# Kernel tuning notes

Hardware: AMD Instinct MI355X
Metric: run time of the kernel (lower is better)

Reference implementation:

```python
import jax, jax.numpy as jnp
import numpy as np
from jax import lax

N_BITS = 4  # init kwarg n_bits
Q_SCALE = 2.0 ** (N_BITS - 1) - 1.0  # signed n-bit levels


def ste_round(x):
    # straight-through rounding (identity gradient)
    return x + lax.stop_gradient(jnp.round(x) - x)


def quant_signed(x):
    # clip to [-1,1], quantize to 2^(n-1)-1 signed levels with STE
    return ste_round(jnp.clip(x, -1.0, 1.0) * Q_SCALE) / Q_SCALE


def qconv(x, w):
    # QuantizeConv: 3x3 stride-1 pad-1 conv with n-bit quantized weights
    return lax.conv_general_dilated(x, quant_signed(w), window_strides=(1, 1),
                                    padding=((1, 1), (1, 1)),
                                    dimension_numbers=('NCHW', 'OIHW', 'NCHW'))


def qact_conv(x, g, b):
    # QuantizeSignedActSBN (conv): per-channel scale/bias then signed quant
    return quant_signed(x * g[None, :, None, None] + b[None, :, None, None])


def qact_fc(x, g, b):
    return quant_signed(x * g[None, :] + b[None, :])


def maxpool2(x):
    return lax.reduce_window(x, -jnp.inf, lax.max, (1, 1, 2, 2), (1, 1, 2, 2), 'VALID')


def setup_inputs() -> dict:
    key = jax.random.key(0)
    ks = jax.random.split(key, 32)
    B = 512
    x = jax.random.normal(ks[0], (B, 3, 32, 32), dtype=jnp.float32)
    chans = [(64, 3), (64, 64), (128, 64), (128, 128), (256, 128), (256, 256)]
    inp = {'x': x}
    ki = 1
    for i, (co, ci) in enumerate(chans, start=1):
        inp[f'w{i}'] = jax.random.normal(ks[ki], (co, ci, 3, 3), dtype=jnp.float32) * 0.05; ki += 1
        inp[f'g{i}'] = jax.random.uniform(ks[ki], (co,), dtype=jnp.float32, minval=0.5, maxval=1.5); ki += 1
        inp[f'b{i}'] = jax.random.normal(ks[ki], (co,), dtype=jnp.float32) * 0.05; ki += 1
    # FC head: 4096 -> 512 -> 10 (torch Linear weight layout [out, in])
    inp['wf1'] = jax.random.normal(ks[ki], (512, 4096), dtype=jnp.float32) * 0.02; ki += 1
    inp['gf1'] = jax.random.uniform(ks[ki], (512,), dtype=jnp.float32, minval=0.5, maxval=1.5); ki += 1
    inp['bf1'] = jax.random.normal(ks[ki], (512,), dtype=jnp.float32) * 0.05; ki += 1
    inp['wf2'] = jax.random.normal(ks[ki], (10, 512), dtype=jnp.float32) * 0.05; ki += 1
    inp['gf2'] = jax.random.uniform(ks[ki], (10,), dtype=jnp.float32, minval=0.5, maxval=1.5); ki += 1
    inp['bf2'] = jax.random.normal(ks[ki], (10,), dtype=jnp.float32) * 0.05; ki += 1
    return inp


def reference(x, w1, g1, b1, w2, g2, b2, w3, g3, b3, w4, g4, b4, w5, g5, b5, w6, g6, b6,
              wf1, gf1, bf1, wf2, gf2, bf2):
    h = jax.nn.relu(qact_conv(qconv(x, w1), g1, b1))
    h = jax.nn.relu(qact_conv(qconv(h, w2), g2, b2))
    h = maxpool2(h)  # 32 -> 16
    h = jax.nn.relu(qact_conv(qconv(h, w3), g3, b3))
    h = jax.nn.relu(qact_conv(qconv(h, w4), g4, b4))
    h = maxpool2(h)  # 16 -> 8
    h = jax.nn.relu(qact_conv(qconv(h, w5), g5, b5))
    h = jax.nn.relu(qact_conv(qconv(h, w6), g6, b6))
    h = maxpool2(h)  # 8 -> 4 => 256*4*4 = 4096
    h = h.reshape(h.shape[0], -1)
    h = jax.nn.relu(qact_fc(h @ quant_signed(wf1).T, gf1, bf1))
    h = qact_fc(h @ quant_signed(wf2).T, gf2, bf2)
    return h
```

## Files before the change

kernel.cpp:

```cpp
#include <hip/hip_runtime.h>


typedef __attribute__((ext_vector_type(4))) int v4i;

#if defined(__has_builtin)
# if __has_builtin(__builtin_amdgcn_sdot4)
#  define HAS_SDOT4 1
# endif
#endif

__device__ __forceinline__ int dot4_i8(int a, int b, int c) {
#ifdef HAS_SDOT4
    return __builtin_amdgcn_sdot4(a, b, c, false);
#else
    c += ((a      ) & 0xff) * (int)(signed char)(b      );
    c += ((a >>  8) & 0xff) * (int)(signed char)(b >>  8);
    c += ((a >> 16) & 0xff) * (int)(signed char)(b >> 16);
    c += ((a >> 24) & 0xff) * (int)(signed char)(b >> 24);
    return c;
#endif
}

__device__ __forceinline__ void gld_lds16(const void* g, void* l) {
    __builtin_amdgcn_global_load_lds(
        (const __attribute__((address_space(1))) unsigned int*)g,
        (__attribute__((address_space(3))) unsigned int*)l, 16, 0, 0);
}

#define O_QW1    0u
#define O_QWF2   4096u
#define O_ZERO   10240u
#define O_QWT2   16384u
#define O_QWT3   65536u
#define O_QWT4   147456u
#define O_QWT5   294912u
#define O_QWT6   589824u
#define O_QWF1   1179648u
#define O_BUFA   3276800u
#define O_BUFB   36831232u

__device__ __forceinline__ signed char quant_w(double v) {
    return (signed char)(int)rint(fmin(fmax(v, -1.0), 1.0) * 7.0);
}

__device__ __forceinline__ void quantw_body(const float* __restrict__ w,
                                            signed char* __restrict__ q, int i, int n) {
    if (i < n) q[i] = quant_w((double)w[i]);
}

__device__ __forceinline__ void quantw_t8p_body(const float* __restrict__ w,
                                                signed char* __restrict__ o,
                                                int CI, int i, int n) {
    if (i < n) {
        const int b  = i & 15;
        const int t  = i >> 4;
        const int rows_per_grp = CI * 36;
        const int grp  = t / rows_per_grp;
        int rr = t - grp * rows_per_grp;
        const int pass = rr / 2304;
        rr -= pass * 2304;
        const int c    = rr / 576;
        const int row  = rr - c * 576;
        const int co_l = row / 9;
        const int tap  = row - co_l * 9;
        const int co = grp * 64 + co_l;
        const int ci = pass * 64 + c * 16 + b;
        o[i] = quant_w((double)w[(co * CI + ci) * 9 + tap]);
    }
}

__device__ __forceinline__ void quantw_fc1_body(const float* __restrict__ w,
                                                signed char* __restrict__ o, int i) {
    if (i < 512 * 4096) {
        int j  = i >> 12;
        int kn = i & 4095;
        int gp = kn >> 8;
        int r  = kn & 255;
        int px = r >> 4;
        int b  = r & 15;
        int ko = (gp * 16 + b) * 16 + px;
        o[i] = quant_w((double)w[j * 4096 + ko]);
    }
}

__global__ __launch_bounds__(256) void prep_k(
    const float* __restrict__ w1,  signed char* __restrict__ qw1,
    const float* __restrict__ wf2, signed char* __restrict__ qwf2,
    const float* __restrict__ w2,  signed char* __restrict__ qwt2,
    const float* __restrict__ w3,  signed char* __restrict__ qwt3,
    const float* __restrict__ w4,  signed char* __restrict__ qwt4,
    const float* __restrict__ w5,  signed char* __restrict__ qwt5,
    const float* __restrict__ w6,  signed char* __restrict__ qwt6,
    const float* __restrict__ wf1, signed char* __restrict__ qwf1,
    unsigned char* __restrict__ zs)
{
    const int blk = blockIdx.x;
    const int t   = threadIdx.x;
    if (blk == 0 && t < 16) ((int4*)zs)[t] = int4{0, 0, 0, 0};
    if      (blk < 7)    quantw_body(w1, qw1, blk * 256 + t, 1728);
    else if (blk < 27)   quantw_body(wf2, qwf2, (blk - 7) * 256 + t, 5120);
    else if (blk < 171)  quantw_t8p_body(w2, qwt2, 64,  (blk - 27)   * 256 + t, 36864);
    else if (blk < 459)  quantw_t8p_body(w3, qwt3, 64,  (blk - 171)  * 256 + t, 73728);
    else if (blk < 1035) quantw_t8p_body(w4, qwt4, 128, (blk - 459)  * 256 + t, 147456);
    else if (blk < 2187) quantw_t8p_body(w5, qwt5, 128, (blk - 1035) * 256 + t, 294912);
    else if (blk < 4491) quantw_t8p_body(w6, qwt6, 256, (blk - 2187) * 256 + t, 589824);
    else                 quantw_fc1_body(wf1, qwf1, (blk - 4491) * 256 + t);
}

#define XSTR 34
#define XPL  (10 * XSTR)
__global__ __launch_bounds__(256) void conv1_k(
    const float* __restrict__ x, const signed char* __restrict__ wq,
    const float* __restrict__ gvec, const float* __restrict__ bvec,
    unsigned char* __restrict__ out)
{
    __shared__ double xs[3 * XPL];
    __shared__ double wd[16 * 27];
    __shared__ __align__(16) unsigned char ob[256 * 16];

    const int tid  = threadIdx.x;
    const int sp   = tid & 63;
    const int cg   = tid >> 6;
    const int img  = blockIdx.x >> 2;
    const int slab = blockIdx.x & 3;
    const int y0s  = slab * 8;
    const int co_base = blockIdx.y * 16;
    const int yb = sp >> 4, xb = sp & 15;
    const int ysl = yb * 2, x0 = xb * 2;

    for (int i = tid; i < 432; i += 256)
        wd[i] = (double)wq[co_base * 27 + i];
    for (int i = tid; i < 3 * XPL; i += 256) {
        int ci = i / XPL, r = i - ci * XPL;
        int ry = r / XSTR, rx = r - ry * XSTR;
        int gy = y0s - 1 + ry, gx = rx - 1;
        double v = 0.0;
        if ((unsigned)gy < 32u && (unsigned)gx < 32u)
            v = (double)x[(img * 3 + ci) * 1024 + gy * 32 + gx];
        xs[i] = v;
    }
    __syncthreads();

    double acc[4][4];
#pragma unroll
    for (int l = 0; l < 4; ++l)
#pragma unroll
        for (int p = 0; p < 4; ++p) acc[l][p] = 0.0;

#pragma unroll
    for (int ci = 0; ci < 3; ++ci) {
        double a[4][4];
#pragma unroll
        for (int iy = 0; iy < 4; ++iy)
#pragma unroll
            for (int ix = 0; ix < 4; ++ix)
                a[iy][ix] = xs[ci * XPL + (ysl + iy) * XSTR + (x0 + ix)];
#pragma unroll
        for (int l = 0; l < 4; ++l) {
            const double* wr = &wd[((cg * 4 + l) * 3 + ci) * 9];
#pragma unroll
            for (int ky = 0; ky < 3; ++ky)
#pragma unroll
                for (int kx = 0; kx < 3; ++kx) {
                    const double wv = wr[ky * 3 + kx];
                    acc[l][0] = fma(wv, a[ky    ][kx    ], acc[l][0]);
                    acc[l][1] = fma(wv, a[ky    ][kx + 1], acc[l][1]);
                    acc[l][2] = fma(wv, a[ky + 1][kx    ], acc[l][2]);
                    acc[l][3] = fma(wv, a[ky + 1][kx + 1], acc[l][3]);
                }
        }
    }

    int qv[4][4];
#pragma unroll
    for (int l = 0; l < 4; ++l) {
        const int co = co_base + cg * 4 + l;
        const double gg  = (double)gvec[co];
        const double bb7 = (double)bvec[co] * 7.0;
#pragma unroll
        for (int p = 0; p < 4; ++p) {
            int qi = (int)rint(fma(acc[l][p], gg, bb7));
            qv[l][p] = qi < 0 ? 0 : (qi > 7 ? 7 : qi);
        }
    }
#pragma unroll
    for (int p = 0; p < 4; ++p) {
        unsigned int wv = (unsigned int)qv[0][p]
                        | ((unsigned int)qv[1][p] << 8)
                        | ((unsigned int)qv[2][p] << 16)
                        | ((unsigned int)qv[3][p] << 24);
        const int r = ysl + (p >> 1), c = x0 + (p & 1);
        const int px = r * 32 + c;
        const int slot = (cg ^ ((px >> 3) & 3) ^ ((px >> 6) & 3)) & 3;
        *(unsigned int*)&ob[px * 16 + slot * 4] = wv;
    }
    __syncthreads();
    {
        uint4 d = *(const uint4*)&ob[tid * 16];
        const int s = (((tid >> 3) & 3) ^ ((tid >> 6) & 3)) & 3;
        unsigned e0 = d.x, e1 = d.y, e2 = d.z, e3 = d.w, t;
        if (s & 1) { t = e0; e0 = e1; e1 = t; t = e2; e2 = e3; e3 = t; }
        if (s & 2) { t = e0; e0 = e2; e2 = t; t = e1; e1 = e3; e3 = t; }
        uint4 o; o.x = e0; o.y = e1; o.z = e2; o.w = e3;
        *(uint4*)&out[(size_t)img * 65536 + (size_t)blockIdx.y * 16384
                      + y0s * 512 + tid * 16] = o;
    }
}

template<int CI, int CO, int H, int W, bool POOL, int IPB, int TPB>
__global__ __launch_bounds__(256, 2) void conv_i8_k(
    const unsigned char* __restrict__ in, const signed char* __restrict__ wt,
    const float* __restrict__ gvec, const float* __restrict__ bvec,
    unsigned char* __restrict__ out, const unsigned char* __restrict__ zs)
{
    constexpr int ATX    = (IPB == 1) ? 18 : 10;
    constexpr int APX    = ATX * ATX;
    constexpr int APLANE = IPB * APX * 16;
    constexpr int WBASE  = 4 * APLANE;
    constexpr int WPLANE = 576 * 16;
    constexpr int NPASS  = CI / 64;
    constexpr int PIN    = CI / 16;
    constexpr int PXI    = H * W;
    constexpr int POUT   = CO / 16;
    constexpr int PXO    = POOL ? (H / 2) * (W / 2) : H * W;
    static_assert(TPB == 1 || (NPASS == 1 && IPB == 1), "TPB>1 needs NPASS==1");

    __shared__ __align__(16) char lds[WBASE + 4 * WPLANE];

    const int tid = threadIdx.x;
    const int l   = tid & 63;
    const int w   = tid >> 6;
    const int n   = l & 15;
    const int q   = l >> 4;

    const int co_base = blockIdx.y * 64;
    const int wy8 = (IPB == 1) ? (w >> 1) * 8 : 0;
    const int wx8 = (IPB == 1) ? (w & 1) * 8 : 0;
    const int tilepx = (IPB == 4) ? w * APX : 0;

    const int ly = ((n >> 3) & 1) * 2 + ((n >> 1) & 1);
    const int lx = ((n >> 2) & 1) * 2 + (n & 1);

    int abase[4], wbase[4];
#pragma unroll
    for (int ps = 0; ps < 4; ++ps) {
        int ay0 = wy8 + (ps >> 1) * 4 + ly;
        int ax0 = wx8 + (ps & 1) * 4 + lx;
        abase[ps] = q * APLANE + (tilepx + ay0 * ATX + ax0) * 16;
    }
#pragma unroll
    for (int cs = 0; cs < 4; ++cs)
        wbase[cs] = WBASE + q * WPLANE + ((cs * 16 + n) * 9) * 16;

    auto stage_act = [&](int img0, int regY0, int regX0, int pass) {
#pragma unroll
        for (int c = 0; c < 4; ++c) {
            const int gp = pass * 4 + c;
            for (int base = 0; base < IPB * APX; base += 256) {
                const int px_g = base + tid;
                if (px_g < IPB * APX) {
                    int tile = 0, px = px_g;
                    if (IPB == 4) { tile = px_g / APX; px = px_g - tile * APX; }
                    const int gy = regY0 - 1 + px / ATX;
                    const int gx = regX0 - 1 + px % ATX;
                    const int bimg = img0 + tile;
                    const void* src =
                        ((unsigned)gy < (unsigned)H && (unsigned)gx < (unsigned)W)
                        ? (const void*)&in[((size_t)(bimg * PIN + gp) * PXI + gy * W + gx) * 16]
                        : (const void*)zs;
                    gld_lds16(src, &lds[c * APLANE + px_g * 16]);
                }
            }
        }
    };
    auto stage_w = [&](int pass) {
        const signed char* wsrc = wt + (size_t)(blockIdx.y * NPASS + pass) * (4 * WPLANE);
#pragma unroll
        for (int base = 0; base < 2304; base += 256)
            gld_lds16(wsrc + (base + tid) * 16, &lds[WBASE + (base + tid) * 16]);
    };
    auto taps = [&](v4i acc[4][4]) {
#pragma unroll
        for (int tap = 0; tap < 9; ++tap) {
            const int toff = ((tap / 3) * ATX + (tap % 3)) * 16;
            v4i bf[4], af[4];
#pragma unroll
            for (int cs = 0; cs < 4; ++cs)
                bf[cs] = *(const v4i*)&lds[wbase[cs] + tap * 16];
#pragma unroll
            for (int ps = 0; ps < 4; ++ps)
                af[ps] = *(const v4i*)&lds[abase[ps] + toff];
#pragma unroll
            for (int ps = 0; ps < 4; ++ps)
#pragma unroll
                for (int cs = 0; cs < 4; ++cs)
                    acc[ps][cs] = __builtin_amdgcn_mfma_i32_16x16x64_i8(
                        af[ps], bf[cs], acc[ps][cs], 0, 0, 0);
        }
    };
    auto epilogue = [&](v4i acc[4][4], int img0, int regY0, int regX0) {
        const int bimg = (IPB == 1) ? img0 : (img0 + w);
#pragma unroll
        for (int cs = 0; cs < 4; ++cs) {
            const int co = co_base + cs * 16 + n;
            const int pl = (co_base >> 4) + cs;
            const double g7 = (double)gvec[co] * (1.0 / 7.0);
            const double b7 = (double)bvec[co] * 7.0;
#pragma unroll
            for (int ps = 0; ps < 4; ++ps) {
                const int Yb = regY0 + wy8 + (ps >> 1) * 4 + (q >> 1) * 2;
                const int Xb = regX0 + wx8 + (ps & 1) * 4 + (q & 1) * 2;
                if (POOL) {
                    int ms = max(max(acc[ps][cs][0], acc[ps][cs][1]),
                                 max(acc[ps][cs][2], acc[ps][cs][3]));
                    int qi = (int)rint(fma((double)ms, g7, b7));
                    qi = qi < 0 ? 0 : (qi > 7 ? 7 : qi);
                    out[((size_t)(bimg * POUT + pl) * PXO + (Yb >> 1) * (W / 2) + (Xb >> 1)) * 16 + n]
                        = (unsigned char)qi;
                } else {
#pragma unroll
                    for (int r = 0; r < 4; ++r) {
                        int qi = (int)rint(fma((double)acc[ps][cs][r], g7, b7));
                        qi = qi < 0 ? 0 : (qi > 7 ? 7 : qi);
                        const int Y = Yb + (r >> 1), X = Xb + (r & 1);
                        out[((size_t)(bimg * POUT + pl) * PXO + Y * W + X) * 16 + n]
                            = (unsigned char)qi;
                    }
                }
            }
        }
    };

    if (TPB == 1) {
        int img = 0, regY0 = 0, regX0 = 0;
        if (IPB == 1) {
            constexpr int rpw = W / 16;
            constexpr int rpi = (H / 16) * rpw;
            img   = blockIdx.x / rpi;
            int r = blockIdx.x % rpi;
            regY0 = (r / rpw) * 16;
            regX0 = (r % rpw) * 16;
        } else {
            img = (int)blockIdx.x * 4;
        }
        v4i acc[4][4];
#pragma unroll
        for (int ps = 0; ps < 4; ++ps)
#pragma unroll
            for (int cs = 0; cs < 4; ++cs) acc[ps][cs] = (v4i)0;

        for (int pass = 0; pass < NPASS; ++pass) {
            __syncthreads();
            stage_act(img, regY0, regX0, pass);
            stage_w(pass);
            __syncthreads();
            taps(acc);
        }
        epilogue(acc, img, regY0, regX0);
    } else {
        stage_w(0);
        for (int tt = 0; tt < TPB; ++tt) {
            const int t = (int)blockIdx.x * TPB + tt;
            int img, regY0 = 0, regX0 = 0;
            if (H == 32) {
                img = t >> 2;
                regY0 = ((t >> 1) & 1) * 16;
                regX0 = (t & 1) * 16;
            } else {
                img = t;
            }
            __syncthreads();
            stage_act(img, regY0, regX0, 0);
            __syncthreads();
            v4i acc[4][4];
#pragma unroll
            for (int ps = 0; ps < 4; ++ps)
#pragma unroll
                for (int cs = 0; cs < 4; ++cs) acc[ps][cs] = (v4i)0;
            taps(acc);
            epilogue(acc, img, regY0, regX0);
        }
    }
}

__global__ __launch_bounds__(256, 2) void fc1_i8_k(
    const unsigned char* __restrict__ h, const signed char* __restrict__ wt,
    const float* __restrict__ gvec, const float* __restrict__ bvec,
    unsigned char* __restrict__ out)
{
    __shared__ int red[4096];
    const int tid = threadIdx.x;
    const int l = tid & 63, w = tid >> 6;
    const int n = l & 15, q = l >> 4;
    const int m0 = blockIdx.x * 32, n0 = blockIdx.y * 32;

    v4i acc[2][2];
#pragma unroll
    for (int a = 0; a < 2; ++a)
#pragma unroll
        for (int b = 0; b < 2; ++b) acc[a][b] = (v4i)0;

    const int kb = w * 1024;
    for (int ks = 0; ks < 16; ++ks) {
        const int k = kb + ks * 64 + q * 16;
        v4i af[2], bf[2];
#pragma unroll
        for (int ms = 0; ms < 2; ++ms)
            af[ms] = *(const v4i*)&h[(m0 + ms * 16 + n) * 4096 + k];
#pragma unroll
        for (int ns = 0; ns < 2; ++ns)
            bf[ns] = *(const v4i*)&wt[(n0 + ns * 16 + n) * 4096 + k];
#pragma unroll
        for (int ms = 0; ms < 2; ++ms)
#pragma unroll
            for (int ns = 0; ns < 2; ++ns)
                acc[ms][ns] = __builtin_amdgcn_mfma_i32_16x16x64_i8(
                    af[ms], bf[ns], acc[ms][ns], 0, 0, 0);
    }

#pragma unroll
    for (int ms = 0; ms < 2; ++ms)
#pragma unroll
        for (int ns = 0; ns < 2; ++ns)
#pragma unroll
            for (int r = 0; r < 4; ++r)
                red[w * 1024 + (ms * 16 + q * 4 + r) * 32 + ns * 16 + n] = acc[ms][ns][r];
    __syncthreads();

#pragma unroll
    for (int j = 0; j < 4; ++j) {
        const int e = tid * 4 + j;
        int s = red[e] + red[1024 + e] + red[2048 + e] + red[3072 + e];
        const int ml = e >> 5, nl = e & 31;
        const int co = n0 + nl;
        double y7 = fma((double)s, (double)gvec[co] * (1.0 / 7.0), (double)bvec[co] * 7.0);
        int qi = (int)rint(y7);
        qi = qi < 0 ? 0 : (qi > 7 ? 7 : qi);
        out[(m0 + ml) * 512 + co] = (unsigned char)qi;
    }
}

__global__ __launch_bounds__(256) void fc2_k(
    const unsigned char* __restrict__ h, const signed char* __restrict__ wq,
    const float* __restrict__ gvec, const float* __restrict__ bvec,
    float* __restrict__ out)
{
    const int gid = blockIdx.x * 256 + threadIdx.x;
    const int b = gid >> 4;
    const int n = gid & 15;
    if (b >= 512 || n >= 10) return;
    const int* hp = (const int*)&h[b * 512];
    const int* wp = (const int*)&wq[n * 512];
    int s = 0;
#pragma unroll 4
    for (int k = 0; k < 128; k += 4) {
        int4 hv = *(const int4*)&hp[k];
        int4 wv = *(const int4*)&wp[k];
        s = dot4_i8(hv.x, wv.x, s);
        s = dot4_i8(hv.y, wv.y, s);
        s = dot4_i8(hv.z, wv.z, s);
        s = dot4_i8(hv.w, wv.w, s);
    }
    double y7 = fma((double)s, (double)gvec[n] * (1.0 / 7.0), (double)bvec[n] * 7.0);
    double r = rint(y7);
    r = fmin(fmax(r, -7.0), 7.0);
    out[b * 10 + n] = (float)(r / 7.0);
}

extern "C" void kernel_launch(void* const* d_in, const int* in_sizes, int n_in,
                              void* d_out, int out_size, void* d_ws, size_t ws_size,
                              hipStream_t stream) {
    const float* x   = (const float*)d_in[0];
    const float* w1  = (const float*)d_in[1];
    const float* g1  = (const float*)d_in[2];
    const float* b1  = (const float*)d_in[3];
    const float* w2  = (const float*)d_in[4];
    const float* g2  = (const float*)d_in[5];
    const float* b2  = (const float*)d_in[6];
    const float* w3  = (const float*)d_in[7];
    const float* g3  = (const float*)d_in[8];
    const float* b3  = (const float*)d_in[9];
    const float* w4  = (const float*)d_in[10];
    const float* g4  = (const float*)d_in[11];
    const float* b4  = (const float*)d_in[12];
    const float* w5  = (const float*)d_in[13];
    const float* g5  = (const float*)d_in[14];
    const float* b5  = (const float*)d_in[15];
    const float* w6  = (const float*)d_in[16];
    const float* g6  = (const float*)d_in[17];
    const float* b6  = (const float*)d_in[18];
    const float* wf1 = (const float*)d_in[19];
    const float* gf1 = (const float*)d_in[20];
    const float* bf1 = (const float*)d_in[21];
    const float* wf2 = (const float*)d_in[22];
    const float* gf2 = (const float*)d_in[23];
    const float* bf2 = (const float*)d_in[24];

    char* ws = (char*)d_ws;
    signed char*   qw1  = (signed char*)(ws + O_QW1);
    signed char*   qwf2 = (signed char*)(ws + O_QWF2);
    unsigned char* zs   = (unsigned char*)(ws + O_ZERO);
    signed char*   qwt2 = (signed char*)(ws + O_QWT2);
    signed char*   qwt3 = (signed char*)(ws + O_QWT3);
    signed char*   qwt4 = (signed char*)(ws + O_QWT4);
    signed char*   qwt5 = (signed char*)(ws + O_QWT5);
    signed char*   qwt6 = (signed char*)(ws + O_QWT6);
    signed char*   qwf1 = (signed char*)(ws + O_QWF1);
    unsigned char* bufA = (unsigned char*)(ws + O_BUFA);
    unsigned char* bufB = (unsigned char*)(ws + O_BUFB);

    hipLaunchKernelGGL(prep_k, dim3(12683), dim3(256), 0, stream,
                       w1, qw1, wf2, qwf2, w2, qwt2, w3, qwt3,
                       w4, qwt4, w5, qwt5, w6, qwt6, wf1, qwf1, zs);

    hipLaunchKernelGGL(conv1_k, dim3(2048, 4), dim3(256), 0, stream, x, qw1, g1, b1, bufA);
    hipLaunchKernelGGL((conv_i8_k<64,  64,  32, 32, true,  1, 4>), dim3(512,  1), dim3(256), 0, stream, bufA, qwt2, g2, b2, bufB, zs);
    hipLaunchKernelGGL((conv_i8_k<64,  128, 16, 16, false, 1, 2>), dim3(256,  2), dim3(256), 0, stream, bufB, qwt3, g3, b3, bufA, zs);
    hipLaunchKernelGGL((conv_i8_k<128, 128, 16, 16, true,  1, 1>), dim3(512,  2), dim3(256), 0, stream, bufA, qwt4, g4, b4, bufB, zs);
    hipLaunchKernelGGL((conv_i8_k<128, 256, 8,  8,  false, 4, 1>), dim3(128,  4), dim3(256), 0, stream, bufB, qwt5, g5, b5, bufA, zs);
    hipLaunchKernelGGL((conv_i8_k<256, 256, 8,  8,  true,  4, 1>), dim3(128,  4), dim3(256), 0, stream, bufA, qwt6, g6, b6, bufB, zs);

    hipLaunchKernelGGL(fc1_i8_k, dim3(16, 16), dim3(256), 0, stream, bufB, qwf1, gf1, bf1, bufA);
    hipLaunchKernelGGL(fc2_k, dim3(32), dim3(256), 0, stream, bufA, qwf2, gf2, bf2, (float*)d_out);
}
```

Before: 254.2 us.

## Double-buffer conv activation staging, merge conv1 channel groups, vectorize fc1 weight quantization

Three separate changes. The fc1 weight quantization now gives each block one row: it does float4 loads, quantizes into LDS, then writes permuted bytes packed four per word, which shrinks the prep grid. conv1 now computes all 64 output channels in one block with a loop over four channel groups, so the input tile is staged once rather than four times, at the cost of fewer blocks. Conv layers that process several tiles per block double-buffer the activation LDS region so the next tile's async load overlaps the current taps, which uses more LDS and may lower occupancy.

```diff
diff --git a/kernel.cpp b/kernel.cpp
--- a/kernel.cpp
+++ b/kernel.cpp
@@ -69,17 +69,39 @@
     }
 }
 
-__device__ __forceinline__ void quantw_fc1_body(const float* __restrict__ w,
-                                                signed char* __restrict__ o, int i) {
-    if (i < 512 * 4096) {
-        int j  = i >> 12;
-        int kn = i & 4095;
-        int gp = kn >> 8;
-        int r  = kn & 255;
-        int px = r >> 4;
-        int b  = r & 15;
-        int ko = (gp * 16 + b) * 16 + px;
-        o[i] = quant_w((double)w[j * 4096 + ko]);
+__device__ __forceinline__ void quantw_fc1_row(const float* __restrict__ w,
+                                               signed char* __restrict__ o,
+                                               int row, int tid,
+                                               unsigned char* __restrict__ sb)
+{
+    const float4* wr = (const float4*)(w + row * 4096);
+    unsigned int* so = (unsigned int*)sb;
+#pragma unroll
+    for (int k = 0; k < 4; ++k) {
+        const int d = k * 256 + tid;
+        float4 v = wr[d];
+        unsigned int pk =
+              ((unsigned int)(unsigned char)quant_w((double)v.x))
+            | ((unsigned int)(unsigned char)quant_w((double)v.y) << 8)
+            | ((unsigned int)(unsigned char)quant_w((double)v.z) << 16)
+            | ((unsigned int)(unsigned char)quant_w((double)v.w) << 24);
+        so[d] = pk;
+    }
+    __syncthreads();
+    unsigned int* og = (unsigned int*)(o + row * 4096);
+#pragma unroll
+    for (int k = 0; k < 4; ++k) {
+        const int od = k * 256 + tid;
+        unsigned int pk = 0;
+#pragma unroll
+        for (int u = 0; u < 4; ++u) {
+            const int kn = od * 4 + u;
+            const int gp = kn >> 8, r = kn & 255;
+            const int px = r >> 4, b = r & 15;
+            const int ko = (gp * 16 + b) * 16 + px;
+            pk |= (unsigned int)sb[ko] << (8 * u);
+        }
+        og[od] = pk;
     }
 }
 
@@ -94,6 +116,7 @@
     const float* __restrict__ wf1, signed char* __restrict__ qwf1,
     unsigned char* __restrict__ zs)
 {
+    __shared__ __align__(16) unsigned char sb[4096];
     const int blk = blockIdx.x;
     const int t   = threadIdx.x;
     if (blk == 0 && t < 16) ((int4*)zs)[t] = int4{0, 0, 0, 0};
@@ -104,7 +127,7 @@
     else if (blk < 1035) quantw_t8p_body(w4, qwt4, 128, (blk - 459)  * 256 + t, 147456);
     else if (blk < 2187) quantw_t8p_body(w5, qwt5, 128, (blk - 1035) * 256 + t, 294912);
     else if (blk < 4491) quantw_t8p_body(w6, qwt6, 256, (blk - 2187) * 256 + t, 589824);
-    else                 quantw_fc1_body(wf1, qwf1, (blk - 4491) * 256 + t);
+    else                 quantw_fc1_row(wf1, qwf1, blk - 4491, t, sb);
 }
 
 #define XSTR 34
@@ -115,8 +138,8 @@
     unsigned char* __restrict__ out)
 {
     __shared__ double xs[3 * XPL];
-    __shared__ double wd[16 * 27];
-    __shared__ __align__(16) unsigned char ob[256 * 16];
+    __shared__ double wd[64 * 27];
+    __shared__ __align__(16) unsigned char ob[2][256 * 16];
 
     const int tid  = threadIdx.x;
     const int sp   = tid & 63;
@@ -124,12 +147,11 @@
     const int img  = blockIdx.x >> 2;
     const int slab = blockIdx.x & 3;
     const int y0s  = slab * 8;
-    const int co_base = blockIdx.y * 16;
     const int yb = sp >> 4, xb = sp & 15;
     const int ysl = yb * 2, x0 = xb * 2;
 
-    for (int i = tid; i < 432; i += 256)
-        wd[i] = (double)wq[co_base * 27 + i];
+    for (int i = tid; i < 1728; i += 256)
+        wd[i] = (double)wq[i];
     for (int i = tid; i < 3 * XPL; i += 256) {
         int ci = i / XPL, r = i - ci * XPL;
         int ry = r / XSTR, rx = r - ry * XSTR;
@@ -141,69 +163,71 @@
     }
     __syncthreads();
 
-    double acc[4][4];
-#pragma unroll
-    for (int l = 0; l < 4; ++l)
-#pragma unroll
-        for (int p = 0; p < 4; ++p) acc[l][p] = 0.0;
-
-#pragma unroll
-    for (int ci = 0; ci < 3; ++ci) {
-        double a[4][4];
-#pragma unroll
-        for (int iy = 0; iy < 4; ++iy)
-#pragma unroll
-            for (int ix = 0; ix < 4; ++ix)
-                a[iy][ix] = xs[ci * XPL + (ysl + iy) * XSTR + (x0 + ix)];
+    for (int cog = 0; cog < 4; ++cog) {
+        double acc[4][4];
+#pragma unroll
+        for (int l = 0; l < 4; ++l)
+#pragma unroll
+            for (int p = 0; p < 4; ++p) acc[l][p] = 0.0;
+
+#pragma unroll
+        for (int ci = 0; ci < 3; ++ci) {
+            double a[4][4];
+#pragma unroll
+            for (int iy = 0; iy < 4; ++iy)
+#pragma unroll
+                for (int ix = 0; ix < 4; ++ix)
+                    a[iy][ix] = xs[ci * XPL + (ysl + iy) * XSTR + (x0 + ix)];
+#pragma unroll
+            for (int l = 0; l < 4; ++l) {
+                const double* wr = &wd[((cog * 16 + cg * 4 + l) * 3 + ci) * 9];
+#pragma unroll
+                for (int ky = 0; ky < 3; ++ky)
+#pragma unroll
+                    for (int kx = 0; kx < 3; ++kx) {
+                        const double wv = wr[ky * 3 + kx];
+                        acc[l][0] = fma(wv, a[ky    ][kx    ], acc[l][0]);
+                        acc[l][1] = fma(wv, a[ky    ][kx + 1], acc[l][1]);
+                        acc[l][2] = fma(wv, a[ky + 1][kx    ], acc[l][2]);
+                        acc[l][3] = fma(wv, a[ky + 1][kx + 1], acc[l][3]);
+                    }
+            }
+        }
+
+        int qv[4][4];
 #pragma unroll
         for (int l = 0; l < 4; ++l) {
-            const double* wr = &wd[((cg * 4 + l) * 3 + ci) * 9];
-#pragma unroll
-            for (int ky = 0; ky < 3; ++ky)
-#pragma unroll
-                for (int kx = 0; kx < 3; ++kx) {
-                    const double wv = wr[ky * 3 + kx];
-                    acc[l][0] = fma(wv, a[ky    ][kx    ], acc[l][0]);
-                    acc[l][1] = fma(wv, a[ky    ][kx + 1], acc[l][1]);
-                    acc[l][2] = fma(wv, a[ky + 1][kx    ], acc[l][2]);
-                    acc[l][3] = fma(wv, a[ky + 1][kx + 1], acc[l][3]);
-                }
-        }
-    }
-
-    int qv[4][4];
-#pragma unroll
-    for (int l = 0; l < 4; ++l) {
-        const int co = co_base + cg * 4 + l;
-        const double gg  = (double)gvec[co];
-        const double bb7 = (double)bvec[co] * 7.0;
+            const int co = cog * 16 + cg * 4 + l;
+            const double gg  = (double)gvec[co];
+            const double bb7 = (double)bvec[co] * 7.0;
+#pragma unroll
+            for (int p = 0; p < 4; ++p) {
+                int qi = (int)rint(fma(acc[l][p], gg, bb7));
+                qv[l][p] = qi < 0 ? 0 : (qi > 7 ? 7 : qi);
+            }
+        }
 #pragma unroll
         for (int p = 0; p < 4; ++p) {
-            int qi = (int)rint(fma(acc[l][p], gg, bb7));
-            qv[l][p] = qi < 0 ? 0 : (qi > 7 ? 7 : qi);
-        }
-    }
-#pragma unroll
-    for (int p = 0; p < 4; ++p) {
-        unsigned int wv = (unsigned int)qv[0][p]
-                        | ((unsigned int)qv[1][p] << 8)
-                        | ((unsigned int)qv[2][p] << 16)
-                        | ((unsigned int)qv[3][p] << 24);
-        const int r = ysl + (p >> 1), c = x0 + (p & 1);
-        const int px = r * 32 + c;
-        const int slot = (cg ^ ((px >> 3) & 3) ^ ((px >> 6) & 3)) & 3;
-        *(unsigned int*)&ob[px * 16 + slot * 4] = wv;
-    }
-    __syncthreads();
-    {
-        uint4 d = *(const uint4*)&ob[tid * 16];
-        const int s = (((tid >> 3) & 3) ^ ((tid >> 6) & 3)) & 3;
-        unsigned e0 = d.x, e1 = d.y, e2 = d.z, e3 = d.w, t;
-        if (s & 1) { t = e0; e0 = e1; e1 = t; t = e2; e2 = e3; e3 = t; }
-        if (s & 2) { t = e0; e0 = e2; e2 = t; t = e1; e1 = e3; e3 = t; }
-        uint4 o; o.x = e0; o.y = e1; o.z = e2; o.w = e3;
-        *(uint4*)&out[(size_t)img * 65536 + (size_t)blockIdx.y * 16384
-                      + y0s * 512 + tid * 16] = o;
+            unsigned int wv = (unsigned int)qv[0][p]
+                            | ((unsigned int)qv[1][p] << 8)
+                            | ((unsigned int)qv[2][p] << 16)
+                            | ((unsigned int)qv[3][p] << 24);
+            const int r = ysl + (p >> 1), c = x0 + (p & 1);
+            const int px = r * 32 + c;
+            const int slot = (cg ^ ((px >> 3) & 3) ^ ((px >> 6) & 3)) & 3;
+            *(unsigned int*)&ob[cog & 1][px * 16 + slot * 4] = wv;
+        }
+        __syncthreads();
+        {
+            uint4 d = *(const uint4*)&ob[cog & 1][tid * 16];
+            const int s = (((tid >> 3) & 3) ^ ((tid >> 6) & 3)) & 3;
+            unsigned e0 = d.x, e1 = d.y, e2 = d.z, e3 = d.w, t;
+            if (s & 1) { t = e0; e0 = e1; e1 = t; t = e2; e2 = e3; e3 = t; }
+            if (s & 2) { t = e0; e0 = e2; e2 = t; t = e1; e1 = e3; e3 = t; }
+            uint4 o; o.x = e0; o.y = e1; o.z = e2; o.w = e3;
+            *(uint4*)&out[(size_t)img * 65536 + (size_t)cog * 16384
+                          + y0s * 512 + tid * 16] = o;
+        }
     }
 }
 
@@ -216,7 +240,9 @@
     constexpr int ATX    = (IPB == 1) ? 18 : 10;
     constexpr int APX    = ATX * ATX;
     constexpr int APLANE = IPB * APX * 16;
-    constexpr int WBASE  = 4 * APLANE;
+    constexpr int AREG   = 4 * APLANE;
+    constexpr int NBUF   = (TPB > 1) ? 2 : 1;
+    constexpr int WBASE  = NBUF * AREG;
     constexpr int WPLANE = 576 * 16;
     constexpr int NPASS  = CI / 64;
     constexpr int PIN    = CI / 16;
@@ -252,7 +278,7 @@
     for (int cs = 0; cs < 4; ++cs)
         wbase[cs] = WBASE + q * WPLANE + ((cs * 16 + n) * 9) * 16;
 
-    auto stage_act = [&](int img0, int regY0, int regX0, int pass) {
+    auto stage_act = [&](int boff, int img0, int regY0, int regX0, int pass) {
 #pragma unroll
         for (int c = 0; c < 4; ++c) {
             const int gp = pass * 4 + c;
@@ -268,7 +294,7 @@
                         ((unsigned)gy < (unsigned)H && (unsigned)gx < (unsigned)W)
                         ? (const void*)&in[((size_t)(bimg * PIN + gp) * PXI + gy * W + gx) * 16]
                         : (const void*)zs;
-                    gld_lds16(src, &lds[c * APLANE + px_g * 16]);
+                    gld_lds16(src, &lds[boff + c * APLANE + px_g * 16]);
                 }
             }
         }
@@ -279,7 +305,7 @@
         for (int base = 0; base < 2304; base += 256)
             gld_lds16(wsrc + (base + tid) * 16, &lds[WBASE + (base + tid) * 16]);
     };
-    auto taps = [&](v4i acc[4][4]) {
+    auto taps = [&](v4i acc[4][4], int boff) {
 #pragma unroll
         for (int tap = 0; tap < 9; ++tap) {
             const int toff = ((tap / 3) * ATX + (tap % 3)) * 16;
@@ -289,7 +315,7 @@
                 bf[cs] = *(const v4i*)&lds[wbase[cs] + tap * 16];
 #pragma unroll
             for (int ps = 0; ps < 4; ++ps)
-                af[ps] = *(const v4i*)&lds[abase[ps] + toff];
+                af[ps] = *(const v4i*)&lds[boff + abase[ps] + toff];
 #pragma unroll
             for (int ps = 0; ps < 4; ++ps)
 #pragma unroll
@@ -351,34 +377,38 @@
 
         for (int pass = 0; pass < NPASS; ++pass) {
             __syncthreads();
-            stage_act(img, regY0, regX0, pass);
+            stage_act(0, img, regY0, regX0, pass);
             stage_w(pass);
             __syncthreads();
-            taps(acc);
+            taps(acc, 0);
         }
         epilogue(acc, img, regY0, regX0);
     } else {
+        auto tilec = [&](int t, int& im, int& ry, int& rx) {
+            if (H == 32) { im = t >> 2; ry = ((t >> 1) & 1) * 16; rx = (t & 1) * 16; }
+            else         { im = t; ry = 0; rx = 0; }
+        };
         stage_w(0);
+        int im0, ry0, rx0;
+        tilec((int)blockIdx.x * TPB, im0, ry0, rx0);
+        stage_act(0, im0, ry0, rx0, 0);
+        __syncthreads();
         for (int tt = 0; tt < TPB; ++tt) {
-            const int t = (int)blockIdx.x * TPB + tt;
-            int img, regY0 = 0, regX0 = 0;
-            if (H == 32) {
-                img = t >> 2;
-                regY0 = ((t >> 1) & 1) * 16;
-                regX0 = (t & 1) * 16;
-            } else {
-                img = t;
+            int imc, ryc, rxc;
+            tilec((int)blockIdx.x * TPB + tt, imc, ryc, rxc);
+            if (tt + 1 < TPB) {
+                int imn, ryn, rxn;
+                tilec((int)blockIdx.x * TPB + tt + 1, imn, ryn, rxn);
+                stage_act(((tt + 1) & 1) * AREG, imn, ryn, rxn, 0);
             }
+            v4i acc[4][4];
+#pragma unroll
+            for (int ps = 0; ps < 4; ++ps)
+#pragma unroll
+                for (int cs = 0; cs < 4; ++cs) acc[ps][cs] = (v4i)0;
+            taps(acc, (tt & 1) * AREG);
+            epilogue(acc, imc, ryc, rxc);
             __syncthreads();
-            stage_act(img, regY0, regX0, 0);
-            __syncthreads();
-            v4i acc[4][4];
-#pragma unroll
-            for (int ps = 0; ps < 4; ++ps)
-#pragma unroll
-                for (int cs = 0; cs < 4; ++cs) acc[ps][cs] = (v4i)0;
-            taps(acc);
-            epilogue(acc, img, regY0, regX0);
         }
     }
 }
@@ -509,11 +539,11 @@
     unsigned char* bufA = (unsigned char*)(ws + O_BUFA);
     unsigned char* bufB = (unsigned char*)(ws + O_BUFB);
 
-    hipLaunchKernelGGL(prep_k, dim3(12683), dim3(256), 0, stream,
+    hipLaunchKernelGGL(prep_k, dim3(5003), dim3(256), 0, stream,
                        w1, qw1, wf2, qwf2, w2, qwt2, w3, qwt3,
                        w4, qwt4, w5, qwt5, w6, qwt6, wf1, qwf1, zs);
 
-    hipLaunchKernelGGL(conv1_k, dim3(2048, 4), dim3(256), 0, stream, x, qw1, g1, b1, bufA);
+    hipLaunchKernelGGL(conv1_k, dim3(2048), dim3(256), 0, stream, x, qw1, g1, b1, bufA);
     hipLaunchKernelGGL((conv_i8_k<64,  64,  32, 32, true,  1, 4>), dim3(512,  1), dim3(256), 0, stream, bufA, qwt2, g2, b2, bufB, zs);
     hipLaunchKernelGGL((conv_i8_k<64,  128, 16, 16, false, 1, 2>), dim3(256,  2), dim3(256), 0, stream, bufB, qwt3, g3, b3, bufA, zs);
     hipLaunchKernelGGL((conv_i8_k<128, 128, 16, 16, true,  1, 1>), dim3(512,  2), dim3(256), 0, stream, bufA, qwt4, g4, b4, bufB, zs);
```

Result: faster. 244.7 us (-3.7%).
